# Performance work log

Measured on AMD Instinct MI355X. Metric: run time of the kernel, lower is better.

## Reference

```python
import jax, jax.numpy as jnp
import numpy as np

L, D, H, DFF, P, B = 10, 512, 8, 1536, 16, 1024
DK = D // H
SQRT_DK = float(np.sqrt(DK))

# board geometry constants (square index -> rank/file/diag)
_pos = np.arange(64)
FILES = _pos % 8
RANKS = _pos // 8
DIAGS = RANKS + FILES
ADIAGS = RANKS - FILES + 7
RIDX = np.clip(RANKS[:, None] - RANKS[None, :], -7, 7) + 7  # [64,64]
FIDX = np.clip(FILES[:, None] - FILES[None, :], -7, 7) + 7  # [64,64]


def setup_inputs() -> dict:
    key = jax.random.key(0)
    ks = iter(jax.random.split(key, 40))
    n = lambda shape, s=0.02: (jax.random.normal(next(ks), shape, jnp.float32) * s)
    inp = {
        'x': jax.random.normal(next(ks), (B, 64, P), jnp.float32),
        'emb_W': n((P, D)), 'emb_b': jnp.zeros((D,), jnp.float32),
        'cls': n((1, 1, D)), 'abs_pos': n((1, 64, D)),
        'file_tab': n((8, D)), 'rank_tab': n((8, D)),
        'diag_tab': n((15, D)), 'anti_tab': n((15, D)),
        'rel_bias': n((L, 15, 15, H)),
        'Wq': n((L, D, D)), 'bq': jnp.zeros((L, D)),
        'Wk': n((L, D, D)), 'bk': jnp.zeros((L, D)),
        'Wv': n((L, D, D)), 'bv': jnp.zeros((L, D)),
        'Wo': n((L, D, D)), 'bo': jnp.zeros((L, D)),
        'ln1_g': jnp.ones((L, D)), 'ln1_b': jnp.zeros((L, D)),
        'ln2_g': jnp.ones((L, D)), 'ln2_b': jnp.zeros((L, D)),
        'W1': n((L, D, 2 * DFF)), 'b1': jnp.zeros((L, 2 * DFF)),
        'W2': n((L, DFF, D)), 'b2': jnp.zeros((L, D)),
        'fln_g': jnp.ones((D,)), 'fln_b': jnp.zeros((D,)),
        'pol_W': n((D, 72)), 'pol_b': jnp.zeros((72,)),
        'v1_W': n((D, D // 2)), 'v1_b': jnp.zeros((D // 2,)),
        'v2_W': n((D // 2, 128)), 'v2_b': jnp.zeros((128,)),
        'v3_W': n((128, 1)), 'v3_b': jnp.zeros((1,)),
    }
    return inp


def _ln(x, g, b):
    m = x.mean(-1, keepdims=True)
    v = ((x - m) ** 2).mean(-1, keepdims=True)
    return (x - m) * jax.lax.rsqrt(v + 1e-5) * g + b


def _gelu(x):
    return jax.nn.gelu(x, approximate=False)  # torch F.gelu default (erf)


def reference(x, emb_W, emb_b, cls, abs_pos, file_tab, rank_tab, diag_tab, anti_tab,
              rel_bias, Wq, bq, Wk, bk, Wv, bv, Wo, bo, ln1_g, ln1_b, ln2_g, ln2_b,
              W1, b1, W2, b2, fln_g, fln_b, pol_W, pol_b,
              v1_W, v1_b, v2_W, v2_b, v3_W, v3_b):
    Bn = x.shape[0]
    # per-square embedding + chess positional encoding
    emb = x @ emb_W + emb_b                                   # [B,64,D]
    pe = abs_pos + file_tab[FILES] + rank_tab[RANKS] + diag_tab[DIAGS] + anti_tab[ADIAGS]
    t = emb + pe
    t = jnp.concatenate([jnp.broadcast_to(cls, (Bn, 1, D)), t], axis=1)  # [B,65,D]
    for i in range(L):
        h = _ln(t, ln1_g[i], ln1_b[i])
        q = (h @ Wq[i] + bq[i]).reshape(Bn, 65, H, DK).transpose(0, 2, 1, 3)
        k = (h @ Wk[i] + bk[i]).reshape(Bn, 65, H, DK).transpose(0, 2, 1, 3)
        v = (h @ Wv[i] + bv[i]).reshape(Bn, 65, H, DK).transpose(0, 2, 1, 3)
        scores = jnp.einsum('bhqd,bhkd->bhqk', q, k) / SQRT_DK
        bias = rel_bias[i][RIDX, FIDX]                        # [64,64,H]
        bias = jnp.pad(bias.transpose(2, 0, 1), ((0, 0), (1, 0), (1, 0)))  # zero bias for CLS
        scores = scores + bias[None]
        a = jax.nn.softmax(scores, axis=-1)
        ctx = jnp.einsum('bhqk,bhkd->bhqd', a, v).transpose(0, 2, 1, 3).reshape(Bn, 65, D)
        t = t + (ctx @ Wo[i] + bo[i])
        h = _ln(t, ln2_g[i], ln2_b[i])
        p = h @ W1[i] + b1[i]
        x1, x2 = jnp.split(p, 2, axis=-1)
        t = t + (_gelu(x1) * x2) @ W2[i] + b2[i]
    t = _ln(t, fln_g, fln_b)
    policy = (t[:, 1:] @ pol_W + pol_b).reshape(Bn, -1)       # [B,4608]
    vh = t[:, 0]                                              # CLS token
    value = jnp.tanh(_gelu(_gelu(vh @ v1_W + v1_b) @ v2_W + v2_b) @ v3_W + v3_b)  # [B,1]
    return policy, value
```

## Files before the change

### kernel.cpp

```cpp
#include <hip/hip_runtime.h>
#include <hip/hip_bf16.h>
#include <math.h>


typedef short short8 __attribute__((ext_vector_type(8)));
typedef float f32x4 __attribute__((ext_vector_type(4)));

#define NLAYER 10
#define DMODEL 512
#define NHEAD 8
#define BATCH 1024
#define SEQ 65

#define WT_QKV   0L
#define WT_WO    7864320L
#define WT_W1    10485760L
#define WT_W2    26214400L
#define WT_BQKV  34078720L
#define WT_BO    34094080L
#define WT_B1    34099200L
#define WT_B2    34129920L
#define WT_POL   34135040L
#define WT_BPOL  34200576L
#define WT_TOTAL 34200704L

__device__ __forceinline__ float bf2f(ushort u){ return __uint_as_float(((unsigned)u)<<16); }
__device__ __forceinline__ ushort f2bf(float f){
  unsigned u = __float_as_uint(f);
  unsigned r = (u + 0x7fffu + ((u>>16)&1u)) >> 16;
  return (ushort)r;
}
__device__ __forceinline__ float gelu_exact(float x){
  return 0.5f*x*(1.0f+erff(x*0.70710678118654752440f));
}
__device__ __forceinline__ void gl16(ushort* lds, const ushort* g){
  __builtin_amdgcn_global_load_lds(
      (const unsigned int __attribute__((address_space(1)))*)g,
      (unsigned int __attribute__((address_space(3)))*)lds,
      16, 0, 0);
}

__global__ void prep_qkv(const float* __restrict__ Wq, const float* __restrict__ Wk,
                         const float* __restrict__ Wv, ushort* __restrict__ wT)
{
  long idx = (long)blockIdx.x*256 + threadIdx.x;
  if(idx >= 7864320L) return;
  int l = (int)(idx/786432L);
  long r = idx - (long)l*786432L;
  int n = (int)(r>>9), k = (int)(r&511);
  float v;
  if(n<512)       v = Wq[(long)l*262144 + (long)k*512 + n];
  else if(n<1024) v = Wk[(long)l*262144 + (long)k*512 + (n-512)];
  else            v = Wv[(long)l*262144 + (long)k*512 + (n-1024)];
  wT[WT_QKV + idx] = f2bf(v);
}
__global__ void prep_wo(const float* __restrict__ Wo, ushort* __restrict__ wT)
{
  long idx = (long)blockIdx.x*256 + threadIdx.x;
  if(idx >= 2621440L) return;
  int l = (int)(idx/262144L);
  long r = idx - (long)l*262144L;
  int n = (int)(r>>9), k = (int)(r&511);
  wT[WT_WO + idx] = f2bf(Wo[(long)l*262144 + (long)k*512 + n]);
}
__global__ void prep_w1(const float* __restrict__ W1, ushort* __restrict__ wT)
{
  long idx = (long)blockIdx.x*256 + threadIdx.x;
  if(idx >= 15728640L) return;
  int l = (int)(idx/1572864L);
  long r = idx - (long)l*1572864L;
  int n = (int)(r>>9), k = (int)(r&511);
  int j = n>>1;
  int src = (n&1) ? 1536+j : j;
  wT[WT_W1 + idx] = f2bf(W1[(long)l*1572864 + (long)k*3072 + src]);
}
__global__ void prep_w2(const float* __restrict__ W2, ushort* __restrict__ wT)
{
  long idx = (long)blockIdx.x*256 + threadIdx.x;
  if(idx >= 7864320L) return;
  int l = (int)(idx/786432L);
  long r = idx - (long)l*786432L;
  int n = (int)(r/1536), k = (int)(r - (long)n*1536);
  wT[WT_W2 + idx] = f2bf(W2[(long)l*786432 + (long)k*512 + n]);
}
__global__ void prep_bias(const float* __restrict__ bq, const float* __restrict__ bk,
                          const float* __restrict__ bv, const float* __restrict__ bo,
                          const float* __restrict__ b1, const float* __restrict__ b2,
                          ushort* __restrict__ wT)
{
  int idx = blockIdx.x*256 + threadIdx.x;
  if(idx >= 56320) return;
  long o = WT_BQKV + idx;
  float v;
  if(o < WT_BO){
    int i = idx;
    int l = i/1536, n = i - l*1536;
    if(n<512) v=bq[l*512+n]; else if(n<1024) v=bk[l*512+n-512]; else v=bv[l*512+n-1024];
  } else if(o < WT_B1){
    int i = (int)(o - WT_BO);
    v = bo[i];
  } else if(o < WT_B2){
    int i = (int)(o - WT_B1);
    int l = i/3072, n = i - l*3072;
    int j=n>>1; int src=(n&1)?1536+j:j;
    v = b1[l*3072+src];
  } else {
    int i = (int)(o - WT_B2);
    v = b2[i];
  }
  wT[o] = f2bf(v);
}
__global__ void prep_pol(const float* __restrict__ pol_W, const float* __restrict__ pol_b,
                         ushort* __restrict__ wT)
{
  int idx = blockIdx.x*256 + threadIdx.x;
  if(idx >= 65536+128) return;
  if(idx < 65536){
    int n = idx>>9, k = idx&511;
    wT[WT_POL + idx] = f2bf(n<72 ? pol_W[k*72+n] : 0.0f);
  } else {
    int n = idx - 65536;
    wT[WT_BPOL + n] = f2bf(n<72 ? pol_b[n] : 0.0f);
  }
}

__global__ __launch_bounds__(256) void embed_kernel(
    const float* __restrict__ x, const float* __restrict__ emb_W,
    const float* __restrict__ emb_b, const float* __restrict__ cls,
    const float* __restrict__ abs_pos, const float* __restrict__ file_tab,
    const float* __restrict__ rank_tab, const float* __restrict__ diag_tab,
    const float* __restrict__ anti_tab, float* __restrict__ t, long xoff)
{
  long tok = (long)blockIdx.x*4 + (threadIdx.x>>6);
  int lane = threadIdx.x&63;
  long b = tok/SEQ;
  int s = (int)(tok - b*SEQ);
  float* out = t + tok*DMODEL;
  if(s==0){
    #pragma unroll
    for(int j=0;j<8;j++){ int d=lane*8+j; out[d]=cls[d]; }
    return;
  }
  int p = s-1;
  int f = p&7, r = p>>3;
  int dg = r+f, ad = r-f+7;
  float xv[16];
  #pragma unroll
  for(int k=0;k<16;k++) xv[k]=x[xoff + (b*64+p)*16+k];
  #pragma unroll
  for(int j=0;j<8;j++){
    int d = lane*8+j;
    float acc = emb_b[d] + abs_pos[p*512+d] + file_tab[f*512+d]
              + rank_tab[r*512+d] + diag_tab[dg*512+d] + anti_tab[ad*512+d];
    #pragma unroll
    for(int k=0;k<16;k++) acc += xv[k]*emb_W[k*512+d];
    out[d]=acc;
  }
}

__global__ __launch_bounds__(256) void ln_kernel(const float* __restrict__ t, ushort* __restrict__ h,
                                                 const float* __restrict__ g, const float* __restrict__ b,
                                                 long goff)
{
  long tok = (long)blockIdx.x*4 + (threadIdx.x>>6);
  int lane = threadIdx.x&63;
  const float* row = t + tok*DMODEL;
  float4 v0 = *reinterpret_cast<const float4*>(row + lane*8);
  float4 v1 = *reinterpret_cast<const float4*>(row + lane*8 + 4);
  float x[8] = {v0.x,v0.y,v0.z,v0.w,v1.x,v1.y,v1.z,v1.w};
  float s=0.f, ss=0.f;
  #pragma unroll
  for(int j=0;j<8;j++){ s+=x[j]; ss+=x[j]*x[j]; }
  #pragma unroll
  for(int off=32;off>=1;off>>=1){ s+=__shfl_down(s,off); ss+=__shfl_down(ss,off); }
  s=__shfl(s,0); ss=__shfl(ss,0);
  float mean = s*(1.0f/512.0f);
  float var  = ss*(1.0f/512.0f) - mean*mean;
  float rs = rsqrtf(fmaxf(var,0.0f) + 1e-5f);
  #pragma unroll
  for(int j=0;j<8;j++){
    int d=lane*8+j;
    h[tok*DMODEL+d] = f2bf((x[j]-mean)*rs*g[goff+d] + b[goff+d]);
  }
}

template<int EPI>
__global__ __launch_bounds__(256,2) void gemm_bt(
    const ushort* __restrict__ A, long lda,
    const ushort* __restrict__ BT,
    const ushort* __restrict__ bias,
    ushort* __restrict__ Cb, float* __restrict__ Cf,
    long ldc, int K)
{
  __shared__ __align__(16) ushort As[128*32];
  __shared__ __align__(16) ushort Bs[128*32];
  const int tid = threadIdx.x;
  const int w = tid>>6, lane = tid&63, q = lane>>4, lr = lane&15;
  const int wm = (w>>1)*64, wn = (w&1)*64;
  const long mBase = (long)blockIdx.y*128, nBase = (long)blockIdx.x*128;

  f32x4 acc[4][4];
  #pragma unroll
  for(int i=0;i<4;i++)
    #pragma unroll
    for(int j=0;j<4;j++) acc[i][j]=(f32x4)(0.0f);

  const int idx0=tid, idx1=tid+256;
  const int ar0=idx0>>2, ac0=(idx0&3)*8;
  const int ar1=idx1>>2, ac1=(idx1&3)*8;

  const ushort* gA0 = A  + (mBase+ar0)*lda     + ac0;
  const ushort* gA1 = A  + (mBase+ar1)*lda     + ac1;
  const ushort* gB0 = BT + (nBase+ar0)*(long)K + ac0;
  const ushort* gB1 = BT + (nBase+ar1)*(long)K + ac1;
  ushort* lA0 = As + idx0*8;
  ushort* lA1 = As + idx1*8;
  ushort* lB0 = Bs + idx0*8;
  ushort* lB1 = Bs + idx1*8;

  for(int k0=0;k0<K;k0+=32){
    __syncthreads();
    gl16(lA0, gA0 + k0);
    gl16(lA1, gA1 + k0);
    gl16(lB0, gB0 + k0);
    gl16(lB1, gB1 + k0);
    __syncthreads();
    short8 af[4], bfr[4];
    #pragma unroll
    for(int mt=0;mt<4;mt++) af[mt]=*reinterpret_cast<const short8*>(As + (wm+mt*16+lr)*32 + q*8);
    #pragma unroll
    for(int nt=0;nt<4;nt++) bfr[nt]=*reinterpret_cast<const short8*>(Bs + (wn+nt*16+lr)*32 + q*8);
    #pragma unroll
    for(int mt=0;mt<4;mt++)
      #pragma unroll
      for(int nt=0;nt<4;nt++)
        acc[mt][nt]=__builtin_amdgcn_mfma_f32_16x16x32_bf16(af[mt],bfr[nt],acc[mt][nt],0,0,0);
  }

  #pragma unroll
  for(int nt=0;nt<4;nt++){
    long n = nBase+wn+nt*16+lr;
    float bv = bf2f(bias[n]);
    #pragma unroll
    for(int mt=0;mt<4;mt++){
      #pragma unroll
      for(int r=0;r<4;r++){
        long m = mBase+wm+mt*16+q*4+r;
        float v = acc[mt][nt][r]+bv;
        if constexpr (EPI==0){
          Cb[m*ldc+n]=f2bf(v);
        } else if constexpr (EPI==1){
          Cf[m*ldc+n]+=v;
        } else if constexpr (EPI==2){
          float partner = __shfl_xor(v,1);
          if(!(lane&1)) Cb[m*ldc + (n>>1)] = f2bf(gelu_exact(v)*partner);
        } else {
          long bl = m/65;
          int p = (int)(m - bl*65) - 1;
          if(p>=0 && n<72) Cf[bl*4608 + (long)p*72 + n] = v;
        }
      }
    }
  }
}

__global__ __launch_bounds__(256) void attn_kernel(const ushort* __restrict__ qkv,
                                                   const float* __restrict__ rel_bias,
                                                   ushort* __restrict__ ctx, int layer)
{
  int bh = blockIdx.x;
  long b = bh>>3;
  int h = bh&7;
  __shared__ __align__(16) ushort QKP[11520];
  __shared__ __align__(16) ushort Vt[64*104];
  __shared__ __align__(16) float  S [65*65];
  __shared__ float relb[225];
  ushort* Qb = QKP;
  ushort* Kb = QKP + 5760;
  ushort* Pb = QKP;
  const long tokBase = b*SEQ;
  const int tid = threadIdx.x;
  const int w = tid>>6, lane = tid&63, q = lane>>4, lr = lane&15;

  for(int idx=tid; idx<SEQ*8; idx+=256){
    int s = idx>>3, c8 = (idx&7)<<3;
    long base = (tokBase+s)*1536 + h*64 + c8;
    *reinterpret_cast<short8*>(&Qb[s*72 + c8]) = *reinterpret_cast<const short8*>(&qkv[base]);
    *reinterpret_cast<short8*>(&Kb[s*72 + c8]) = *reinterpret_cast<const short8*>(&qkv[base+512]);
    short8 v = *reinterpret_cast<const short8*>(&qkv[base+1024]);
    #pragma unroll
    for(int j=0;j<8;j++) Vt[(c8+j)*104 + s] = (ushort)v[j];
  }
  for(int idx=tid; idx<64*32; idx+=256){
    int d = idx>>5, s = 65+(idx&31);
    Vt[d*104 + s] = 0;
  }
  if(tid<225) relb[tid] = rel_bias[((long)layer*225 + tid)*8 + h];
  __syncthreads();

  for(int tt=w; tt<25; tt+=4){
    int mt = tt/5, nt = tt - mt*5;
    f32x4 acc = (f32x4)(0.0f);
    #pragma unroll
    for(int ks=0;ks<2;ks++){
      short8 af = *reinterpret_cast<const short8*>(&Qb[(mt*16+lr)*72 + ks*32 + q*8]);
      short8 bf = *reinterpret_cast<const short8*>(&Kb[(nt*16+lr)*72 + ks*32 + q*8]);
      acc = __builtin_amdgcn_mfma_f32_16x16x32_bf16(af, bf, acc, 0,0,0);
    }
    int col = nt*16 + lr;
    if(col < SEQ){
      #pragma unroll
      for(int r=0;r<4;r++){
        int row = mt*16 + q*4 + r;
        if(row < SEQ) S[row*65 + col] = acc[r]*0.125f;
      }
    }
  }
  __syncthreads();

  {
    int grp = tid>>2, sub = tid&3;
    for(int qi=grp; qi<SEQ; qi+=64){
      float* srow = S + qi*65;
      int pq = qi-1;
      float mx = -1e30f;
      for(int k=sub;k<SEQ;k+=4){
        float s = srow[k];
        if(qi>0 && k>0){
          int pk = k-1;
          int ridx = (pq>>3)-(pk>>3)+7, fidx = (pq&7)-(pk&7)+7;
          s += relb[ridx*15+fidx];
        }
        srow[k] = s;
        mx = fmaxf(mx, s);
      }
      mx = fmaxf(mx, __shfl_xor(mx,1));
      mx = fmaxf(mx, __shfl_xor(mx,2));
      float sum = 0.f;
      for(int k=sub;k<SEQ;k+=4){ float e = __expf(srow[k]-mx); srow[k]=e; sum+=e; }
      sum += __shfl_xor(sum,1);
      sum += __shfl_xor(sum,2);
      float inv = 1.0f/sum;
      ushort* prow = Pb + qi*104;
      for(int k=sub;k<SEQ;k+=4) prow[k] = f2bf(srow[k]*inv);
      for(int k=SEQ+sub;k<96;k+=4) prow[k] = 0;
    }
  }
  __syncthreads();

  for(int tt=w; tt<20; tt+=4){
    int mt = tt>>2, nt = tt&3;
    f32x4 acc = (f32x4)(0.0f);
    #pragma unroll
    for(int ks=0;ks<3;ks++){
      short8 af = *reinterpret_cast<const short8*>(&Pb[(mt*16+lr)*104 + ks*32 + q*8]);
      short8 bf = *reinterpret_cast<const short8*>(&Vt[(nt*16+lr)*104 + ks*32 + q*8]);
      acc = __builtin_amdgcn_mfma_f32_16x16x32_bf16(af, bf, acc, 0,0,0);
    }
    int col = nt*16 + lr;
    #pragma unroll
    for(int r=0;r<4;r++){
      int row = mt*16 + q*4 + r;
      if(row < SEQ)
        ctx[(tokBase+row)*512 + h*64 + col] = f2bf(acc[r]);
    }
  }
}

__global__ __launch_bounds__(256) void value_kernel(const ushort* __restrict__ h,
                                                    const float* __restrict__ v1_W, const float* __restrict__ v1_b,
                                                    const float* __restrict__ v2_W, const float* __restrict__ v2_b,
                                                    const float* __restrict__ v3_W, const float* __restrict__ v3_b,
                                                    float* __restrict__ out, long b0)
{
  long bl = blockIdx.x;
  int tid = threadIdx.x;
  __shared__ float vh[512], a1[256], a2[128];
  const ushort* hrow = h + bl*SEQ*DMODEL;
  for(int d=tid; d<512; d+=256) vh[d]=bf2f(hrow[d]);
  __syncthreads();
  {
    float acc = v1_b[tid];
    for(int k=0;k<512;k++) acc += vh[k]*v1_W[k*256+tid];
    a1[tid]=gelu_exact(acc);
  }
  __syncthreads();
  if(tid<128){
    float acc = v2_b[tid];
    for(int k=0;k<256;k++) acc += a1[k]*v2_W[k*128+tid];
    a2[tid]=gelu_exact(acc);
  }
  __syncthreads();
  if(tid==0){
    float acc = v3_b[0];
    for(int k=0;k<128;k++) acc += a2[k]*v3_W[k];
    out[(long)BATCH*4608 + b0 + bl] = tanhf(acc);
  }
}

extern "C" void kernel_launch(void* const* d_in, const int* in_sizes, int n_in,
                              void* d_out, int out_size, void* d_ws, size_t ws_size,
                              hipStream_t stream)
{
  const float* x        = (const float*)d_in[0];
  const float* emb_W    = (const float*)d_in[1];
  const float* emb_b    = (const float*)d_in[2];
  const float* cls      = (const float*)d_in[3];
  const float* abs_pos  = (const float*)d_in[4];
  const float* file_tab = (const float*)d_in[5];
  const float* rank_tab = (const float*)d_in[6];
  const float* diag_tab = (const float*)d_in[7];
  const float* anti_tab = (const float*)d_in[8];
  const float* rel_bias = (const float*)d_in[9];
  const float* Wq  = (const float*)d_in[10];
  const float* bq  = (const float*)d_in[11];
  const float* Wk  = (const float*)d_in[12];
  const float* bk  = (const float*)d_in[13];
  const float* Wv  = (const float*)d_in[14];
  const float* bv  = (const float*)d_in[15];
  const float* Wo  = (const float*)d_in[16];
  const float* bo  = (const float*)d_in[17];
  const float* ln1_g = (const float*)d_in[18];
  const float* ln1_b = (const float*)d_in[19];
  const float* ln2_g = (const float*)d_in[20];
  const float* ln2_b = (const float*)d_in[21];
  const float* W1  = (const float*)d_in[22];
  const float* b1  = (const float*)d_in[23];
  const float* W2  = (const float*)d_in[24];
  const float* b2  = (const float*)d_in[25];
  const float* fln_g = (const float*)d_in[26];
  const float* fln_b = (const float*)d_in[27];
  const float* pol_W = (const float*)d_in[28];
  const float* pol_b = (const float*)d_in[29];
  const float* v1_W  = (const float*)d_in[30];
  const float* v1_b  = (const float*)d_in[31];
  const float* v2_W  = (const float*)d_in[32];
  const float* v2_b  = (const float*)d_in[33];
  const float* v3_W  = (const float*)d_in[34];
  const float* v3_b  = (const float*)d_in[35];
  float* out = (float*)d_out;

  int nchunk = 4;
  if(ws_size >= (size_t)477345792) nchunk = 1;
  else if(ws_size >= (size_t)272873472) nchunk = 2;
  const int bch = BATCH / nchunk;
  const long mch = (long)bch * SEQ;

  char* ws = (char*)d_ws;
  float*  t    = (float*)ws;  ws += (size_t)mch*DMODEL*4;
  ushort* h    = (ushort*)ws; ws += (size_t)mch*DMODEL*2;
  ushort* buf1 = (ushort*)ws; ws += (size_t)mch*1536*2;
  ushort* wT   = (ushort*)ws; ws += (size_t)WT_TOTAL*2;
  (void)ws_size; (void)in_sizes; (void)n_in; (void)out_size;

  prep_qkv<<<(7864320+255)/256,256,0,stream>>>(Wq,Wk,Wv,wT);
  prep_wo <<<(2621440+255)/256,256,0,stream>>>(Wo,wT);
  prep_w1 <<<(15728640+255)/256,256,0,stream>>>(W1,wT);
  prep_w2 <<<(7864320+255)/256,256,0,stream>>>(W2,wT);
  prep_bias<<<(56320+255)/256,256,0,stream>>>(bq,bk,bv,bo,b1,b2,wT);
  prep_pol <<<(65664+255)/256,256,0,stream>>>(pol_W,pol_b,wT);

  const int gy = (int)(mch/128);
  const int lng = (int)(mch/4);
  for(int c=0;c<nchunk;c++){
    long b0 = (long)c*bch;
    embed_kernel<<<lng,256,0,stream>>>(x, emb_W, emb_b, cls, abs_pos,
                                      file_tab, rank_tab, diag_tab, anti_tab, t, b0*64*16);
    for(int l=0;l<NLAYER;l++){
      ln_kernel<<<lng,256,0,stream>>>(t, h, ln1_g, ln1_b, l*512);
      gemm_bt<0><<<dim3(12,gy),256,0,stream>>>(h, 512, wT+WT_QKV+(long)l*786432,
                                                wT+WT_BQKV+l*1536, buf1, nullptr, 1536, 512);
      attn_kernel<<<bch*NHEAD,256,0,stream>>>(buf1, rel_bias, h, l);
      gemm_bt<1><<<dim3(4,gy),256,0,stream>>>(h, 512, wT+WT_WO+(long)l*262144,
                                               wT+WT_BO+l*512, nullptr, t, 512, 512);
      ln_kernel<<<lng,256,0,stream>>>(t, h, ln2_g, ln2_b, l*512);
      gemm_bt<2><<<dim3(24,gy),256,0,stream>>>(h, 512, wT+WT_W1+(long)l*1572864,
                                                wT+WT_B1+l*3072, buf1, nullptr, 1536, 512);
      gemm_bt<1><<<dim3(4,gy),256,0,stream>>>(buf1, 1536, wT+WT_W2+(long)l*786432,
                                               wT+WT_B2+l*512, nullptr, t, 512, 1536);
    }
    ln_kernel<<<lng,256,0,stream>>>(t, h, fln_g, fln_b, 0);
    gemm_bt<3><<<dim3(1,gy),256,0,stream>>>(h, 512, wT+WT_POL,
                                            wT+WT_BPOL, nullptr, out + b0*4608, 0, 512);
    value_kernel<<<bch,256,0,stream>>>(h, v1_W, v1_b, v2_W, v2_b, v3_W, v3_b, out, b0);
  }
}
```

Measured before the change: 12.51 ms.

## Double GEMM K-tile to 64 and swizzle workgroups across XCDs

The bf16 MFMA GEMM now stages 64-wide K slices of A and B in LDS instead of 32, which halves the number of barrier pairs per output tile and issues more loads per sync. Workgroup IDs are also remapped so that consecutive tiles land on the same XCD, with the aim of improving L2 reuse of shared A/B panels. The cost is doubled LDS use per block (32KB), which may limit occupancy, and a 64-element row stride in LDS that could raise bank conflicts on the fragment reads.

New measurement: 12.44 ms. No clear change (-0.6%).

```diff
diff --git a/kernel.cpp b/kernel.cpp
--- a/kernel.cpp
+++ b/kernel.cpp
@@ -38,6 +38,12 @@
       (const unsigned int __attribute__((address_space(1)))*)g,
       (unsigned int __attribute__((address_space(3)))*)lds,
       16, 0, 0);
+}
+__device__ __forceinline__ int xcd_swizzle(int orig, int nwg){
+  int q8 = nwg>>3, r8 = nwg&7;
+  int xcd = orig&7, off = orig>>3;
+  int base = (xcd<r8) ? xcd*(q8+1) : r8*(q8+1) + (xcd-r8)*q8;
+  return base + off;
 }
 
 __global__ void prep_qkv(const float* __restrict__ Wq, const float* __restrict__ Wk,
@@ -192,12 +198,17 @@
     ushort* __restrict__ Cb, float* __restrict__ Cf,
     long ldc, int K)
 {
-  __shared__ __align__(16) ushort As[128*32];
-  __shared__ __align__(16) ushort Bs[128*32];
+  __shared__ __align__(16) ushort As[128*64];
+  __shared__ __align__(16) ushort Bs[128*64];
   const int tid = threadIdx.x;
   const int w = tid>>6, lane = tid&63, q = lane>>4, lr = lane&15;
   const int wm = (w>>1)*64, wn = (w&1)*64;
-  const long mBase = (long)blockIdx.y*128, nBase = (long)blockIdx.x*128;
+
+  const int nwg  = (int)(gridDim.x*gridDim.y);
+  const int orig = (int)(blockIdx.y*gridDim.x + blockIdx.x);
+  const int wgid = xcd_swizzle(orig, nwg);
+  const int bxx  = wgid % (int)gridDim.x, byy = wgid / (int)gridDim.x;
+  const long mBase = (long)byy*128, nBase = (long)bxx*128;
 
   f32x4 acc[4][4];
   #pragma unroll
@@ -205,36 +216,33 @@
     #pragma unroll
     for(int j=0;j<4;j++) acc[i][j]=(f32x4)(0.0f);
 
-  const int idx0=tid, idx1=tid+256;
-  const int ar0=idx0>>2, ac0=(idx0&3)*8;
-  const int ar1=idx1>>2, ac1=(idx1&3)*8;
-
-  const ushort* gA0 = A  + (mBase+ar0)*lda     + ac0;
-  const ushort* gA1 = A  + (mBase+ar1)*lda     + ac1;
-  const ushort* gB0 = BT + (nBase+ar0)*(long)K + ac0;
-  const ushort* gB1 = BT + (nBase+ar1)*(long)K + ac1;
-  ushort* lA0 = As + idx0*8;
-  ushort* lA1 = As + idx1*8;
-  ushort* lB0 = Bs + idx0*8;
-  ushort* lB1 = Bs + idx1*8;
-
-  for(int k0=0;k0<K;k0+=32){
+  const int ar = tid>>3, ac = (tid&7)*8;
+  const ushort* gA = A  + (mBase+ar)*lda     + ac;
+  const ushort* gB = BT + (nBase+ar)*(long)K + ac;
+  ushort* lA = As + tid*8;
+  ushort* lB = Bs + tid*8;
+
+  for(int k0=0;k0<K;k0+=64){
     __syncthreads();
-    gl16(lA0, gA0 + k0);
-    gl16(lA1, gA1 + k0);
-    gl16(lB0, gB0 + k0);
-    gl16(lB1, gB1 + k0);
+    #pragma unroll
+    for(int i=0;i<4;i++){
+      gl16(lA + i*2048, gA + (long)(i*32)*lda + k0);
+      gl16(lB + i*2048, gB + (long)(i*32)*K   + k0);
+    }
     __syncthreads();
-    short8 af[4], bfr[4];
-    #pragma unroll
-    for(int mt=0;mt<4;mt++) af[mt]=*reinterpret_cast<const short8*>(As + (wm+mt*16+lr)*32 + q*8);
-    #pragma unroll
-    for(int nt=0;nt<4;nt++) bfr[nt]=*reinterpret_cast<const short8*>(Bs + (wn+nt*16+lr)*32 + q*8);
-    #pragma unroll
-    for(int mt=0;mt<4;mt++)
+    #pragma unroll
+    for(int ks=0;ks<2;ks++){
+      short8 af[4], bfr[4];
       #pragma unroll
-      for(int nt=0;nt<4;nt++)
-        acc[mt][nt]=__builtin_amdgcn_mfma_f32_16x16x32_bf16(af[mt],bfr[nt],acc[mt][nt],0,0,0);
+      for(int mt=0;mt<4;mt++) af[mt]=*reinterpret_cast<const short8*>(As + (wm+mt*16+lr)*64 + ks*32 + q*8);
+      #pragma unroll
+      for(int nt=0;nt<4;nt++) bfr[nt]=*reinterpret_cast<const short8*>(Bs + (wn+nt*16+lr)*64 + ks*32 + q*8);
+      #pragma unroll
+      for(int mt=0;mt<4;mt++)
+        #pragma unroll
+        for(int nt=0;nt<4;nt++)
+          acc[mt][nt]=__builtin_amdgcn_mfma_f32_16x16x32_bf16(af[mt],bfr[nt],acc[mt][nt],0,0,0);
+    }
   }
 
   #pragma unroll
```
